# Kernel optimization log

Measured on AMD Instinct MI355X. Metric: run time of the kernel, lower is better.

## Reference

```python
import jax, jax.numpy as jnp
import numpy as np

B, C, H, W = 32, 3, 224, 224
P = 16
D = 768
NH = 12
HD = D // NH
DFF = 3072
L = 12
MAXLEN = 256
S = (H // P) * (W // P)  # 196 patches
EPS = 1e-5


def setup_inputs() -> dict:
    key = jax.random.key(0)
    ks = jax.random.split(key, 10)
    r = lambda k, shp, s=0.02: jax.random.normal(k, shp, jnp.float32) * s
    return {
        "x": jax.random.normal(ks[0], (B, C, H, W), jnp.float32),
        "bn_gamma": jnp.ones((C,), jnp.float32),
        "bn_beta": jnp.zeros((C,), jnp.float32),
        "bn_mean": jnp.zeros((C,), jnp.float32),
        "bn_var": jnp.ones((C,), jnp.float32),
        "proj_w": r(ks[1], (P * P * 3, D)),
        "proj_b": jnp.zeros((D,), jnp.float32),
        "cls_w": r(ks[2], (1, D)),
        "Wq": r(ks[3], (L, D, D)),
        "Wk": r(ks[4], (L, D, D)),
        "Wv": r(ks[5], (L, D, D)),
        "fc1_w": r(ks[6], (L, D, DFF)),
        "fc1_b": jnp.zeros((L, DFF), jnp.float32),
        "fc2_w": r(ks[7], (L, DFF, D)),
        "fc2_b": jnp.zeros((L, D), jnp.float32),
        "ln1_g": jnp.ones((L, D), jnp.float32),
        "ln1_b": jnp.zeros((L, D), jnp.float32),
        "ln2_g": jnp.ones((L, D), jnp.float32),
        "ln2_b": jnp.zeros((L, D), jnp.float32),
    }


def _pos_encoding(max_len, d):
    # Faithful to source: exponent is 2*i/d where i is the EVEN index itself.
    pos = jnp.arange(max_len, dtype=jnp.float32)[:, None]
    i = jnp.arange(0, d, 2, dtype=jnp.float32)[None, :]
    ang = pos / (10000.0 ** (2.0 * i / d))
    pe = jnp.zeros((max_len, d), jnp.float32)
    pe = pe.at[:, 0::2].set(jnp.sin(ang))
    pe = pe.at[:, 1::2].set(jnp.cos(ang))
    return pe


def _layernorm(x, g, b):
    m = jnp.mean(x, axis=-1, keepdims=True)
    v = jnp.mean((x - m) ** 2, axis=-1, keepdims=True)
    return (x - m) * jax.lax.rsqrt(v + EPS) * g + b


def reference(x, bn_gamma, bn_beta, bn_mean, bn_var, proj_w, proj_b, cls_w,
              Wq, Wk, Wv, fc1_w, fc1_b, fc2_w, fc2_b,
              ln1_g, ln1_b, ln2_g, ln2_b):
    b = x.shape[0]
    # BatchNorm2d (inference mode, running stats)
    xb = (x - bn_mean[None, :, None, None]) * jax.lax.rsqrt(bn_var[None, :, None, None] + EPS)
    xb = xb * bn_gamma[None, :, None, None] + bn_beta[None, :, None, None]
    # Patchify (nn.Unfold order: channel-major within each patch) -> [B, S, C*P*P]
    patches = xb.reshape(b, C, H // P, P, W // P, P)
    patches = patches.transpose(0, 2, 4, 1, 3, 5).reshape(b, S, C * P * P)
    h = patches @ proj_w + proj_b  # [B, S, D]
    cls = jnp.broadcast_to(cls_w[None], (b, 1, D))
    h = jnp.concatenate([cls, h], axis=1)  # [B, S+1, D]
    pe = _pos_encoding(MAXLEN, D)
    h = h + pe[None, : S + 1, :]
    scale = 1.0 / jnp.sqrt(jnp.float32(HD))
    n = S + 1
    for l in range(L):
        q = (h @ Wq[l]).reshape(b, n, NH, HD).transpose(0, 2, 1, 3)
        k = (h @ Wk[l]).reshape(b, n, NH, HD).transpose(0, 2, 1, 3)
        v = (h @ Wv[l]).reshape(b, n, NH, HD).transpose(0, 2, 1, 3)
        scores = jnp.einsum("bhqd,bhkd->bhqk", q, k) * scale
        attn = jax.nn.softmax(scores, axis=-1)
        att = jnp.einsum("bhqk,bhkd->bhqd", attn, v)  # [B, NH, n, HD]
        # Source bug replicated: direct view [B,NH,n,HD] -> [B,n,D] (no head transpose)
        att = att.reshape(b, n, D)
        h1 = _layernorm(h + att, ln1_g[l], ln1_b[l])
        ff = jax.nn.relu(h1 @ fc1_w[l] + fc1_b[l]) @ fc2_w[l] + fc2_b[l]
        h = _layernorm(h1 + ff, ln2_g[l], ln2_b[l])
    return h[:, 0, :]
```

## Files before the change

### kernel.cpp

```cpp
#include <hip/hip_runtime.h>

typedef unsigned short u16;
typedef unsigned int u32;
typedef __bf16 bf16x8 __attribute__((ext_vector_type(8)));
typedef float f32x4 __attribute__((ext_vector_type(4)));
typedef u16 u16x8 __attribute__((ext_vector_type(8)));

#define NB 32
#define ND 768
#define NTOK 197
#define NROWS (NB * NTOK)
#define NPATCH 196
#define PROWS (NB * NPATCH)
#define NHD 12
#define NDFF 3072
#define NLAY 12
#define NQKV 2304

static __device__ __forceinline__ u16 f2b(float f) {
  u32 u = __builtin_bit_cast(u32, f);
  u32 r = u + 0x7FFFu + ((u >> 16) & 1u);
  return (u16)(r >> 16);
}
static __device__ __forceinline__ float b2f(u16 u) {
  u32 x = ((u32)u) << 16;
  return __builtin_bit_cast(float, x);
}

static __device__ __forceinline__ float wsum(float v) {
#pragma unroll
  for (int off = 32; off > 0; off >>= 1) v += __shfl_xor(v, off);
  return v;
}

static __device__ __forceinline__ void stage16(const u16* g, u16* l) {
  __builtin_amdgcn_global_load_lds((const __attribute__((address_space(1))) void*)g,
                                   (__attribute__((address_space(3))) void*)l, 16, 0, 0);
}

__global__ void pe_kernel(float* __restrict__ pe) {
  int idx = blockIdx.x * 256 + threadIdx.x;
  if (idx >= NTOK * ND) return;
  int t = idx / ND, d = idx % ND;
  int i = d & ~1;
  float e = (2.0f * (float)i) / (float)ND;
  float denom = powf(10000.0f, e);
  float ang = (float)t / denom;
  pe[idx] = (d & 1) ? cosf(ang) : sinf(ang);
}

__global__ void patch_kernel(const float* __restrict__ x,
                             const float* __restrict__ bng, const float* __restrict__ bnb,
                             const float* __restrict__ bnm, const float* __restrict__ bnv,
                             u16* __restrict__ out) {
  int idx = blockIdx.x * 256 + threadIdx.x;
  if (idx >= PROWS * 96) return;
  int row = idx / 96, c8 = (idx % 96) * 8;
  int b = row / NPATCH, s = row % NPATCH;
  int ph = s / 14, pw = s % 14;
  int c = c8 / 256, rr = c8 % 256;
  int py = rr / 16, px0 = rr % 16;
  const float* xp =
      x + (((size_t)(b * 3 + c) * 224) + ph * 16 + py) * 224 + pw * 16 + px0;
  float scale = rsqrtf(bnv[c] + 1e-5f) * bng[c];
  float sub = bnm[c], add = bnb[c];
  u16x8 o;
#pragma unroll
  for (int j = 0; j < 8; j++) o[j] = f2b((xp[j] - sub) * scale + add);
  *reinterpret_cast<u16x8*>(out + (size_t)idx * 8) = o;
}

__global__ void cls_kernel(const float* __restrict__ cls_w, const float* __restrict__ pe,
                           u16* __restrict__ hb) {
  int idx = blockIdx.x * 256 + threadIdx.x;
  if (idx >= NB * ND) return;
  int b = idx / ND, d = idx % ND;
  hb[(size_t)(b * NTOK) * ND + d] = f2b(cls_w[d] + pe[d]);
}

__global__ __launch_bounds__(256) void transpose_cvt(const float* __restrict__ src,
                                                     u16* __restrict__ dst, int R, int C) {
  __shared__ float tile[32][33];
  int tx = threadIdx.x, ty = threadIdx.y;
  int c0 = blockIdx.x * 32, r0 = blockIdx.y * 32;
#pragma unroll
  for (int i = ty; i < 32; i += 8) {
    int r = r0 + i, c = c0 + tx;
    tile[i][tx] = (r < R && c < C) ? src[(size_t)r * C + c] : 0.f;
  }
  __syncthreads();
#pragma unroll
  for (int i = ty; i < 32; i += 8) {
    int c = c0 + i, r = r0 + tx;
    if (r < R && c < C) dst[(size_t)c * R + r] = f2b(tile[tx][i]);
  }
}

__global__ __launch_bounds__(512) void transpose_layer(
    const float* __restrict__ Wq, const float* __restrict__ Wk, const float* __restrict__ Wv,
    const float* __restrict__ f1, const float* __restrict__ f2,
    u16* __restrict__ wqkvt, u16* __restrict__ fc1t, u16* __restrict__ fc2t) {
  int idx = blockIdx.x;
  const float* src;
  u16* dst;
  int C, R, rt, ct;
  if (idx < 432) {
    int z = idx / 144, loc = idx % 144;
    src = z == 0 ? Wq : (z == 1 ? Wk : Wv);
    dst = wqkvt + (size_t)z * ND * ND;
    R = 768; C = 768; rt = loc / 12; ct = loc % 12;
  } else if (idx < 1008) {
    int loc = idx - 432;
    src = f1; dst = fc1t; R = 768; C = 3072; rt = loc / 48; ct = loc % 48;
  } else {
    int loc = idx - 1008;
    src = f2; dst = fc2t; R = 3072; C = 768; rt = loc / 12; ct = loc % 12;
  }
  __shared__ float tile[64][65];
  const int l2 = threadIdx.x & 31, rp = threadIdx.x >> 5;
  const int r0 = rt * 64, c0 = ct * 64;
#pragma unroll
  for (int i = rp; i < 64; i += 16) {
    float2 v = *reinterpret_cast<const float2*>(src + (size_t)(r0 + i) * C + c0 + l2 * 2);
    tile[i][l2 * 2] = v.x;
    tile[i][l2 * 2 + 1] = v.y;
  }
  __syncthreads();
#pragma unroll
  for (int j = rp; j < 64; j += 16) {
    u32 o = (u32)f2b(tile[l2 * 2][j]) | ((u32)f2b(tile[l2 * 2 + 1][j]) << 16);
    *reinterpret_cast<u32*>(dst + (size_t)(c0 + j) * R + r0 + l2 * 2) = o;
  }
}

template <int MODE>
__global__ __launch_bounds__(512, 4) void gemm2(const u16* __restrict__ A,
                                                const u16* __restrict__ Bt,
                                                const float* __restrict__ bias,
                                                const float* __restrict__ pe,
                                                u16* __restrict__ Cb,
                                                int M, int N, int K, int lda, int nby) {
  __shared__ u16 smem[36864];
  const int tid = threadIdx.x;
  const int w = tid >> 6, l = tid & 63;
  const int lr = l & 15, lg = l >> 4;
  const int wr = w >> 1, wc = w & 1;

  const int nwg = gridDim.x;
  const int q8 = nwg >> 3, r8 = nwg & 7;
  const int xcd = blockIdx.x & 7, sidx = blockIdx.x >> 3;
  const int swz = (xcd < r8 ? xcd * (q8 + 1) : r8 * (q8 + 1) + (xcd - r8) * q8) + sidx;
  const int m0 = (swz / nby) * 256, n0 = (swz % nby) * 128;

  A += (size_t)blockIdx.z * K;
  Bt += (size_t)blockIdx.z * K;

  const int srow = l >> 2;
  const int scol = (((l & 3) ^ ((l >> 2) & 3) ^ ((l >> 4) & 3))) * 8;
  int raA0 = m0 + 32 * w + srow;
  int raA1 = raA0 + 16;
  raA0 = raA0 < M ? raA0 : M - 1;
  raA1 = raA1 < M ? raA1 : M - 1;
  const int rbB = n0 + 16 * w + srow;
  const u16* pA0 = A + (size_t)raA0 * lda + scol;
  const u16* pA1 = A + (size_t)raA1 * lda + scol;
  const u16* pB = Bt + (size_t)rbB * lda + scol;
  const int dsgA0 = (2 * w) * 512;
  const int dsgA1 = (2 * w + 1) * 512;
  const int dsgB = 8192 + w * 512;

  const int xo = ((lg ^ (lr & 3) ^ ((lr >> 2) & 3))) * 8;
  const int aoff = (wr * 64 + lr) * 32 + xo;
  const int boff = 8192 + (wc * 64 + lr) * 32 + xo;

  f32x4 acc[4][4] = {};
  const int nk = K >> 5;

#define BARF                           \
  {                                    \
    __builtin_amdgcn_sched_barrier(0); \
    __builtin_amdgcn_s_barrier();      \
    asm volatile("" ::: "memory");     \
    __builtin_amdgcn_sched_barrier(0); \
  }
#define VMW(N) asm volatile("s_waitcnt vmcnt(" #N ")" ::: "memory");

  stage16(pA0, smem + dsgA0);
  stage16(pA1, smem + dsgA1);
  stage16(pB, smem + dsgB);
  stage16(pA0 + 32, smem + 12288 + dsgA0);
  stage16(pA1 + 32, smem + 12288 + dsgA1);
  stage16(pB + 32, smem + 12288 + dsgB);
  VMW(3);
  BARF;

  int cur = 0;
  for (int t = 0; t < nk; ++t) {
    const u16* sb = smem + cur * 12288;
    int c2 = cur + 2;
    if (c2 >= 3) c2 -= 3;
    const bool more2 = (t + 2) < nk;
    if (more2) {
      u16* db = smem + c2 * 12288;
      const int ko = (t + 2) * 32;
      stage16(pA0 + ko, db + dsgA0);
      stage16(pA1 + ko, db + dsgA1);
      stage16(pB + ko, db + dsgB);
    }
    bf16x8 ar[4], br[4];
#pragma unroll
    for (int n = 0; n < 4; ++n) br[n] = *(const bf16x8*)(sb + boff + n * 512);
#pragma unroll
    for (int m = 0; m < 4; ++m) ar[m] = *(const bf16x8*)(sb + aoff + m * 512);
    __builtin_amdgcn_s_setprio(1);
#pragma unroll
    for (int m = 0; m < 4; ++m) {
#pragma unroll
      for (int n = 0; n < 4; ++n)
        acc[m][n] = __builtin_amdgcn_mfma_f32_16x16x32_bf16(ar[m], br[n], acc[m][n], 0, 0, 0);
    }
    __builtin_amdgcn_s_setprio(0);
    if (more2) {
      VMW(3);
    } else if (t + 1 < nk) {
      VMW(0);
    }
    if (t + 1 < nk) BARF;
    cur = cur == 2 ? 0 : cur + 1;
  }

  const size_t zoff = (size_t)blockIdx.z * (size_t)M * (size_t)N;
#pragma unroll
  for (int m = 0; m < 4; ++m) {
    const int rowb = m0 + wr * 64 + m * 16 + lg * 4;
#pragma unroll
    for (int n = 0; n < 4; ++n) {
      const int col = n0 + wc * 64 + n * 16 + lr;
      float bval = (MODE == 0 || MODE == 2) ? bias[col] : 0.f;
#pragma unroll
      for (int r = 0; r < 4; ++r) {
        const int row = rowb + r;
        if (row < M) {
          float v = acc[m][n][r] + bval;
          if (MODE == 2) v = fmaxf(v, 0.f);
          if (MODE == 0) {
            int b = row / NPATCH, t = 1 + row % NPATCH;
            float val = v + pe[(size_t)t * ND + col];
            Cb[(size_t)(b * NTOK + t) * ND + col] = f2b(val);
          } else if (MODE == 4) {
            Cb[zoff + (size_t)row * N + col] = f2b(v);
          } else {
            Cb[(size_t)row * N + col] = f2b(v);
          }
        }
      }
    }
  }
}

__global__ __launch_bounds__(256) void attn_kernel(const u16* __restrict__ qkv,
                                                   u16* __restrict__ att) {
  const int b = blockIdx.x, h = blockIdx.y;
  const int tid = threadIdx.x;
  const int wave = tid >> 6, lane = tid & 63;
  const int lr = lane & 15, lg = lane >> 4;
  __shared__ u16 Vt[64][232];
  __shared__ u16 Pl[4][16][232];

  const size_t bbase = (size_t)(b * NTOK) * NQKV + h * 64;

  for (int idx = tid; idx < NTOK * 8; idx += 256) {
    int k2 = idx >> 3, d0 = (idx & 7) * 8;
    u16x8 v = *reinterpret_cast<const u16x8*>(qkv + bbase + (size_t)k2 * NQKV + 1536 + d0);
#pragma unroll
    for (int j = 0; j < 8; j++) Vt[d0 + j][k2] = v[j];
  }
  for (int idx = tid; idx < 64 * 35; idx += 256) {
    int d = idx / 35, k2 = 197 + idx % 35;
    Vt[d][k2] = 0;
  }
  for (int idx = tid; idx < 4 * 16 * 24; idx += 256) {
    int w = idx / (16 * 24), rr = (idx / 24) % 16, c = 208 + idx % 24;
    Pl[w][rr][c] = 0;
  }
  __syncthreads();

  for (int mt = wave; mt < 13; mt += 4) {
    int qrow = mt * 16 + lr;
    if (qrow > 196) qrow = 196;
    bf16x8 af[2];
#pragma unroll
    for (int ks = 0; ks < 2; ks++)
      af[ks] =
          *reinterpret_cast<const bf16x8*>(qkv + bbase + (size_t)qrow * NQKV + ks * 32 + lg * 8);

    f32x4 sf[13];
#pragma unroll
    for (int nt = 0; nt < 13; nt++) {
      int krow = nt * 16 + lr;
      if (krow > 196) krow = 196;
      f32x4 z = {0.f, 0.f, 0.f, 0.f};
#pragma unroll
      for (int ks = 0; ks < 2; ks++) {
        bf16x8 bf_ = *reinterpret_cast<const bf16x8*>(qkv + bbase + (size_t)krow * NQKV + 768 +
                                                      ks * 32 + lg * 8);
        z = __builtin_amdgcn_mfma_f32_16x16x32_bf16(af[ks], bf_, z, 0, 0, 0);
      }
      sf[nt] = z;
    }

    float sm[4];
#pragma unroll
    for (int r = 0; r < 4; r++) {
      float mx = -1e30f;
#pragma unroll
      for (int nt = 0; nt < 13; nt++) {
        int col = nt * 16 + lr;
        float val = (col < NTOK) ? sf[nt][r] * 0.125f : -1e30f;
        sf[nt][r] = val;
        mx = fmaxf(mx, val);
      }
#pragma unroll
      for (int off = 1; off < 16; off <<= 1) mx = fmaxf(mx, __shfl_xor(mx, off));
      float sum = 0.f;
#pragma unroll
      for (int nt = 0; nt < 13; nt++) {
        float pv = __expf(sf[nt][r] - mx);
        sum += pv;
        Pl[wave][lg * 4 + r][nt * 16 + lr] = f2b(pv);
      }
#pragma unroll
      for (int off = 1; off < 16; off <<= 1) sum += __shfl_xor(sum, off);
      sm[r] = sum;
    }

#pragma unroll
    for (int dt = 0; dt < 4; dt++) {
      f32x4 o = {0.f, 0.f, 0.f, 0.f};
#pragma unroll
      for (int ks = 0; ks < 7; ks++) {
        bf16x8 pa = *reinterpret_cast<const bf16x8*>(&Pl[wave][lr][ks * 32 + lg * 8]);
        bf16x8 vv = *reinterpret_cast<const bf16x8*>(&Vt[dt * 16 + lr][ks * 32 + lg * 8]);
        o = __builtin_amdgcn_mfma_f32_16x16x32_bf16(pa, vv, o, 0, 0, 0);
      }
#pragma unroll
      for (int r = 0; r < 4; r++) {
        int q = mt * 16 + lg * 4 + r;
        if (q < NTOK)
          att[(size_t)b * (NTOK * ND) + ((size_t)(h * NTOK + q)) * 64 + dt * 16 + lr] =
              f2b(o[r] / sm[r]);
      }
    }
  }
}

__global__ __launch_bounds__(384) void ln_kernel(const u16* __restrict__ xa,
                                                 const u16* __restrict__ xb,
                                                 const float* __restrict__ gw,
                                                 const float* __restrict__ bw,
                                                 u16* __restrict__ yb) {
  int row = blockIdx.x, tid = threadIdx.x;
  size_t p2 = (size_t)row * 384 + tid;
  u32 aa = reinterpret_cast<const u32*>(xa)[p2];
  u32 bb = reinterpret_cast<const u32*>(xb)[p2];
  float v0 = b2f((u16)(aa & 0xffff)) + b2f((u16)(bb & 0xffff));
  float v1 = b2f((u16)(aa >> 16)) + b2f((u16)(bb >> 16));
  __shared__ float red[8], red2[8];
  float s = wsum(v0 + v1);
  if ((tid & 63) == 0) red[tid >> 6] = s;
  __syncthreads();
  float mean = (red[0] + red[1] + red[2] + red[3] + red[4] + red[5]) * (1.f / 768.f);
  float d0 = v0 - mean, d1 = v1 - mean;
  float q = wsum(d0 * d0 + d1 * d1);
  if ((tid & 63) == 0) red2[tid >> 6] = q;
  __syncthreads();
  float inv =
      rsqrtf((red2[0] + red2[1] + red2[2] + red2[3] + red2[4] + red2[5]) * (1.f / 768.f) + 1e-5f);
  int d = tid * 2;
  float o0 = d0 * inv * gw[d] + bw[d];
  float o1 = d1 * inv * gw[d + 1] + bw[d + 1];
  reinterpret_cast<u32*>(yb)[p2] = (u32)f2b(o0) | ((u32)f2b(o1) << 16);
}

__global__ __launch_bounds__(384) void ln_fuse2(const u16* __restrict__ h1b,
                                                const u16* __restrict__ parts,
                                                const float* __restrict__ fb,
                                                const float* __restrict__ gw,
                                                const float* __restrict__ bw,
                                                u16* __restrict__ yb) {
  const size_t PS2 = (size_t)NROWS * ND / 2;
  int row = blockIdx.x, tid = threadIdx.x;
  size_t p2 = (size_t)row * 384 + tid;
  u32 aa = reinterpret_cast<const u32*>(h1b)[p2];
  const u32* pp = reinterpret_cast<const u32*>(parts);
  u32 q0 = pp[p2], q1 = pp[PS2 + p2], q2 = pp[2 * PS2 + p2];
  int d = tid * 2;
  float v0 = b2f((u16)(aa & 0xffff)) + b2f((u16)(q0 & 0xffff)) + b2f((u16)(q1 & 0xffff)) +
             b2f((u16)(q2 & 0xffff)) + fb[d];
  float v1 = b2f((u16)(aa >> 16)) + b2f((u16)(q0 >> 16)) + b2f((u16)(q1 >> 16)) +
             b2f((u16)(q2 >> 16)) + fb[d + 1];
  __shared__ float red[8], red2[8];
  float s = wsum(v0 + v1);
  if ((tid & 63) == 0) red[tid >> 6] = s;
  __syncthreads();
  float mean = (red[0] + red[1] + red[2] + red[3] + red[4] + red[5]) * (1.f / 768.f);
  float d0 = v0 - mean, d1 = v1 - mean;
  float q = wsum(d0 * d0 + d1 * d1);
  if ((tid & 63) == 0) red2[tid >> 6] = q;
  __syncthreads();
  float inv =
      rsqrtf((red2[0] + red2[1] + red2[2] + red2[3] + red2[4] + red2[5]) * (1.f / 768.f) + 1e-5f);
  float o0 = d0 * inv * gw[d] + bw[d];
  float o1 = d1 * inv * gw[d + 1] + bw[d + 1];
  reinterpret_cast<u32*>(yb)[p2] = (u32)f2b(o0) | ((u32)f2b(o1) << 16);
}

__global__ void outcopy_kernel(const u16* __restrict__ hb, float* __restrict__ out) {
  int idx = blockIdx.x * 256 + threadIdx.x;
  if (idx >= NB * ND) return;
  int b = idx / ND, d = idx % ND;
  out[idx] = b2f(hb[(size_t)(b * NTOK) * ND + d]);
}

extern "C" void kernel_launch(void* const* d_in, const int* in_sizes, int n_in, void* d_out,
                              int out_size, void* d_ws, size_t ws_size, hipStream_t stream) {
  const float* x = (const float*)d_in[0];
  const float* bng = (const float*)d_in[1];
  const float* bnb = (const float*)d_in[2];
  const float* bnm = (const float*)d_in[3];
  const float* bnv = (const float*)d_in[4];
  const float* proj_w = (const float*)d_in[5];
  const float* proj_b = (const float*)d_in[6];
  const float* cls_w = (const float*)d_in[7];
  const float* Wq = (const float*)d_in[8];
  const float* Wk = (const float*)d_in[9];
  const float* Wv = (const float*)d_in[10];
  const float* fc1_w = (const float*)d_in[11];
  const float* fc1_b = (const float*)d_in[12];
  const float* fc2_w = (const float*)d_in[13];
  const float* fc2_b = (const float*)d_in[14];
  const float* ln1_g = (const float*)d_in[15];
  const float* ln1_b = (const float*)d_in[16];
  const float* ln2_g = (const float*)d_in[17];
  const float* ln2_b = (const float*)d_in[18];

  char* wp = (char*)d_ws;
  auto carve = [&](size_t bytes) -> char* {
    char* r = wp;
    wp += (bytes + 255) & ~(size_t)255;
    return r;
  };
  float* pe = (float*)carve((size_t)NTOK * ND * 4);
  u16* patches = (u16*)carve((size_t)PROWS * ND * 2);
  u16* projwt = (u16*)carve((size_t)ND * ND * 2);
  u16* wqkvt = (u16*)carve((size_t)NQKV * ND * 2);
  u16* fc1t = (u16*)carve((size_t)ND * NDFF * 2);
  u16* fc2t = (u16*)carve((size_t)ND * NDFF * 2);
  u16* hb = (u16*)carve((size_t)NROWS * ND * 2);
  u16* h1b = (u16*)carve((size_t)NROWS * ND * 2);
  char* uni = carve(3 * (size_t)NROWS * ND * 2);
  u16* qkvb = (u16*)uni;
  u16* parts = (u16*)uni;
  u16* att = (u16*)carve((size_t)NROWS * ND * 2);
  u16* ffb = (u16*)carve((size_t)NROWS * NDFF * 2);
  if ((size_t)(wp - (char*)d_ws) > ws_size) return;

  pe_kernel<<<(NTOK * ND + 255) / 256, 256, 0, stream>>>(pe);
  patch_kernel<<<(PROWS * 96 + 255) / 256, 256, 0, stream>>>(x, bng, bnb, bnm, bnv, patches);
  transpose_cvt<<<dim3(24, 24), dim3(32, 8), 0, stream>>>(proj_w, projwt, ND, ND);
  gemm2<0><<<dim3(150, 1, 1), 512, 0, stream>>>(patches, projwt, proj_b, pe, hb, PROWS, ND, ND,
                                                ND, 6);
  cls_kernel<<<(NB * ND + 255) / 256, 256, 0, stream>>>(cls_w, pe, hb);

  for (int l = 0; l < NLAY; ++l) {
    size_t wo = (size_t)l * ND * ND;
    transpose_layer<<<1584, 512, 0, stream>>>(Wq + wo, Wk + wo, Wv + wo,
                                              fc1_w + (size_t)l * ND * NDFF,
                                              fc2_w + (size_t)l * NDFF * ND, wqkvt, fc1t, fc2t);
    gemm2<1><<<dim3(450, 1, 1), 512, 0, stream>>>(hb, wqkvt, nullptr, nullptr, qkvb, NROWS, NQKV,
                                                  ND, ND, 18);
    attn_kernel<<<dim3(NB, NHD), 256, 0, stream>>>(qkvb, att);
    ln_kernel<<<NROWS, 384, 0, stream>>>(hb, att, ln1_g + l * ND, ln1_b + l * ND, h1b);
    gemm2<2><<<dim3(600, 1, 1), 512, 0, stream>>>(h1b, fc1t, fc1_b + l * NDFF, nullptr, ffb,
                                                  NROWS, NDFF, ND, ND, 24);
    gemm2<4><<<dim3(150, 1, 3), 512, 0, stream>>>(ffb, fc2t, nullptr, nullptr, parts, NROWS, ND,
                                                  1024, NDFF, 6);
    ln_fuse2<<<NROWS, 384, 0, stream>>>(h1b, parts, fc2_b + l * ND, ln2_g + l * ND, ln2_b + l * ND,
                                        hb);
  }
  outcopy_kernel<<<(NB * ND + 255) / 256, 256, 0, stream>>>(hb, (float*)d_out);
}
```

Before: 2.218 ms.

## Fold next-layer weight transpose into QKV GEMM grid and use wave-per-row layernorm

The per-layer weight transpose/convert kernel becomes extra workgroups appended to the QKV GEMM launch, which prepare the next layer's weights into a double-buffered set. This removes one launch per layer and lets transpose work overlap GEMM tail occupancy. Both layernorm kernels now give each 64-lane wave a whole row, so block-level shared-memory reductions and barriers go away. The cost is twice the workspace for transposed weights, and the transpose blocks compete with GEMM blocks for the same CUs.

```diff
diff --git a/kernel.cpp b/kernel.cpp
--- a/kernel.cpp
+++ b/kernel.cpp
@@ -96,11 +96,11 @@
   }
 }
 
-__global__ __launch_bounds__(512) void transpose_layer(
-    const float* __restrict__ Wq, const float* __restrict__ Wk, const float* __restrict__ Wv,
-    const float* __restrict__ f1, const float* __restrict__ f2,
-    u16* __restrict__ wqkvt, u16* __restrict__ fc1t, u16* __restrict__ fc2t) {
-  int idx = blockIdx.x;
+static __device__ __forceinline__ void transpose_body(
+    int idx, const float* __restrict__ Wq, const float* __restrict__ Wk,
+    const float* __restrict__ Wv, const float* __restrict__ f1, const float* __restrict__ f2,
+    u16* __restrict__ wqkvt, u16* __restrict__ fc1t, u16* __restrict__ fc2t, void* smemraw,
+    int tid) {
   const float* src;
   u16* dst;
   int C, R, rt, ct;
@@ -116,8 +116,8 @@
     int loc = idx - 1008;
     src = f2; dst = fc2t; R = 3072; C = 768; rt = loc / 12; ct = loc % 12;
   }
-  __shared__ float tile[64][65];
-  const int l2 = threadIdx.x & 31, rp = threadIdx.x >> 5;
+  float(*tile)[65] = (float(*)[65])smemraw;
+  const int l2 = tid & 31, rp = tid >> 5;
   const int r0 = rt * 64, c0 = ct * 64;
 #pragma unroll
   for (int i = rp; i < 64; i += 16) {
@@ -133,20 +133,33 @@
   }
 }
 
-template <int MODE>
-__global__ __launch_bounds__(512, 4) void gemm2(const u16* __restrict__ A,
-                                                const u16* __restrict__ Bt,
-                                                const float* __restrict__ bias,
-                                                const float* __restrict__ pe,
-                                                u16* __restrict__ Cb,
-                                                int M, int N, int K, int lda, int nby) {
+__global__ __launch_bounds__(512) void transpose_layer(
+    const float* __restrict__ Wq, const float* __restrict__ Wk, const float* __restrict__ Wv,
+    const float* __restrict__ f1, const float* __restrict__ f2,
+    u16* __restrict__ wqkvt, u16* __restrict__ fc1t, u16* __restrict__ fc2t) {
+  __shared__ float tile[64][65];
+  transpose_body(blockIdx.x, Wq, Wk, Wv, f1, f2, wqkvt, fc1t, fc2t, tile, threadIdx.x);
+}
+
+template <int MODE, bool TR>
+__global__ __launch_bounds__(512, 4) void gemm2(
+    const u16* __restrict__ A, const u16* __restrict__ Bt, const float* __restrict__ bias,
+    const float* __restrict__ pe, u16* __restrict__ Cb, int M, int N, int K, int lda, int nby,
+    int ngx, const float* __restrict__ tWq, const float* __restrict__ tWk,
+    const float* __restrict__ tWv, const float* __restrict__ tf1, const float* __restrict__ tf2,
+    u16* __restrict__ twqkv, u16* __restrict__ tfc1, u16* __restrict__ tfc2) {
   __shared__ u16 smem[36864];
+  if (TR && (int)blockIdx.x >= ngx) {
+    transpose_body(blockIdx.x - ngx, tWq, tWk, tWv, tf1, tf2, twqkv, tfc1, tfc2, smem,
+                   threadIdx.x);
+    return;
+  }
   const int tid = threadIdx.x;
   const int w = tid >> 6, l = tid & 63;
   const int lr = l & 15, lg = l >> 4;
   const int wr = w >> 1, wc = w & 1;
 
-  const int nwg = gridDim.x;
+  const int nwg = ngx;
   const int q8 = nwg >> 3, r8 = nwg & 7;
   const int xcd = blockIdx.x & 7, sidx = blockIdx.x >> 3;
   const int swz = (xcd < r8 ? xcd * (q8 + 1) : r8 * (q8 + 1) + (xcd - r8) * q8) + sidx;
@@ -354,65 +367,90 @@
   }
 }
 
-__global__ __launch_bounds__(384) void ln_kernel(const u16* __restrict__ xa,
+__global__ __launch_bounds__(256) void ln_kernel(const u16* __restrict__ xa,
                                                  const u16* __restrict__ xb,
                                                  const float* __restrict__ gw,
                                                  const float* __restrict__ bw,
                                                  u16* __restrict__ yb) {
-  int row = blockIdx.x, tid = threadIdx.x;
-  size_t p2 = (size_t)row * 384 + tid;
-  u32 aa = reinterpret_cast<const u32*>(xa)[p2];
-  u32 bb = reinterpret_cast<const u32*>(xb)[p2];
-  float v0 = b2f((u16)(aa & 0xffff)) + b2f((u16)(bb & 0xffff));
-  float v1 = b2f((u16)(aa >> 16)) + b2f((u16)(bb >> 16));
-  __shared__ float red[8], red2[8];
-  float s = wsum(v0 + v1);
-  if ((tid & 63) == 0) red[tid >> 6] = s;
-  __syncthreads();
-  float mean = (red[0] + red[1] + red[2] + red[3] + red[4] + red[5]) * (1.f / 768.f);
-  float d0 = v0 - mean, d1 = v1 - mean;
-  float q = wsum(d0 * d0 + d1 * d1);
-  if ((tid & 63) == 0) red2[tid >> 6] = q;
-  __syncthreads();
-  float inv =
-      rsqrtf((red2[0] + red2[1] + red2[2] + red2[3] + red2[4] + red2[5]) * (1.f / 768.f) + 1e-5f);
-  int d = tid * 2;
-  float o0 = d0 * inv * gw[d] + bw[d];
-  float o1 = d1 * inv * gw[d + 1] + bw[d + 1];
-  reinterpret_cast<u32*>(yb)[p2] = (u32)f2b(o0) | ((u32)f2b(o1) << 16);
-}
-
-__global__ __launch_bounds__(384) void ln_fuse2(const u16* __restrict__ h1b,
+  int row = blockIdx.x * 4 + (threadIdx.x >> 6);
+  int lane = threadIdx.x & 63;
+  size_t base = (size_t)row * 384;
+  float v0[6], v1[6];
+  float s = 0.f;
+#pragma unroll
+  for (int i = 0; i < 6; i++) {
+    size_t j = base + lane + 64 * i;
+    u32 aa = reinterpret_cast<const u32*>(xa)[j];
+    u32 bb = reinterpret_cast<const u32*>(xb)[j];
+    v0[i] = b2f((u16)(aa & 0xffff)) + b2f((u16)(bb & 0xffff));
+    v1[i] = b2f((u16)(aa >> 16)) + b2f((u16)(bb >> 16));
+    s += v0[i] + v1[i];
+  }
+  s = wsum(s);
+  float mean = s * (1.f / 768.f);
+  float q = 0.f;
+#pragma unroll
+  for (int i = 0; i < 6; i++) {
+    float d0 = v0[i] - mean, d1 = v1[i] - mean;
+    q += d0 * d0 + d1 * d1;
+  }
+  q = wsum(q);
+  float inv = rsqrtf(q * (1.f / 768.f) + 1e-5f);
+#pragma unroll
+  for (int i = 0; i < 6; i++) {
+    int j = lane + 64 * i;
+    float2 g = reinterpret_cast<const float2*>(gw)[j];
+    float2 bb = reinterpret_cast<const float2*>(bw)[j];
+    float o0 = (v0[i] - mean) * inv * g.x + bb.x;
+    float o1 = (v1[i] - mean) * inv * g.y + bb.y;
+    reinterpret_cast<u32*>(yb)[base + j] = (u32)f2b(o0) | ((u32)f2b(o1) << 16);
+  }
+}
+
+__global__ __launch_bounds__(256) void ln_fuse2(const u16* __restrict__ h1b,
                                                 const u16* __restrict__ parts,
                                                 const float* __restrict__ fb,
                                                 const float* __restrict__ gw,
                                                 const float* __restrict__ bw,
                                                 u16* __restrict__ yb) {
   const size_t PS2 = (size_t)NROWS * ND / 2;
-  int row = blockIdx.x, tid = threadIdx.x;
-  size_t p2 = (size_t)row * 384 + tid;
-  u32 aa = reinterpret_cast<const u32*>(h1b)[p2];
-  const u32* pp = reinterpret_cast<const u32*>(parts);
-  u32 q0 = pp[p2], q1 = pp[PS2 + p2], q2 = pp[2 * PS2 + p2];
-  int d = tid * 2;
-  float v0 = b2f((u16)(aa & 0xffff)) + b2f((u16)(q0 & 0xffff)) + b2f((u16)(q1 & 0xffff)) +
-             b2f((u16)(q2 & 0xffff)) + fb[d];
-  float v1 = b2f((u16)(aa >> 16)) + b2f((u16)(q0 >> 16)) + b2f((u16)(q1 >> 16)) +
-             b2f((u16)(q2 >> 16)) + fb[d + 1];
-  __shared__ float red[8], red2[8];
-  float s = wsum(v0 + v1);
-  if ((tid & 63) == 0) red[tid >> 6] = s;
-  __syncthreads();
-  float mean = (red[0] + red[1] + red[2] + red[3] + red[4] + red[5]) * (1.f / 768.f);
-  float d0 = v0 - mean, d1 = v1 - mean;
-  float q = wsum(d0 * d0 + d1 * d1);
-  if ((tid & 63) == 0) red2[tid >> 6] = q;
-  __syncthreads();
-  float inv =
-      rsqrtf((red2[0] + red2[1] + red2[2] + red2[3] + red2[4] + red2[5]) * (1.f / 768.f) + 1e-5f);
-  float o0 = d0 * inv * gw[d] + bw[d];
-  float o1 = d1 * inv * gw[d + 1] + bw[d + 1];
-  reinterpret_cast<u32*>(yb)[p2] = (u32)f2b(o0) | ((u32)f2b(o1) << 16);
+  int row = blockIdx.x * 4 + (threadIdx.x >> 6);
+  int lane = threadIdx.x & 63;
+  size_t base = (size_t)row * 384;
+  float v0[6], v1[6];
+  float s = 0.f;
+#pragma unroll
+  for (int i = 0; i < 6; i++) {
+    size_t j = base + lane + 64 * i;
+    u32 aa = reinterpret_cast<const u32*>(h1b)[j];
+    const u32* pp = reinterpret_cast<const u32*>(parts);
+    u32 q0 = pp[j], q1 = pp[PS2 + j], q2 = pp[2 * PS2 + j];
+    float2 fbv = reinterpret_cast<const float2*>(fb)[lane + 64 * i];
+    v0[i] = b2f((u16)(aa & 0xffff)) + b2f((u16)(q0 & 0xffff)) + b2f((u16)(q1 & 0xffff)) +
+            b2f((u16)(q2 & 0xffff)) + fbv.x;
+    v1[i] = b2f((u16)(aa >> 16)) + b2f((u16)(q0 >> 16)) + b2f((u16)(q1 >> 16)) +
+            b2f((u16)(q2 >> 16)) + fbv.y;
+    s += v0[i] + v1[i];
+  }
+  s = wsum(s);
+  float mean = s * (1.f / 768.f);
+  float q = 0.f;
+#pragma unroll
+  for (int i = 0; i < 6; i++) {
+    float d0 = v0[i] - mean, d1 = v1[i] - mean;
+    q += d0 * d0 + d1 * d1;
+  }
+  q = wsum(q);
+  float inv = rsqrtf(q * (1.f / 768.f) + 1e-5f);
+#pragma unroll
+  for (int i = 0; i < 6; i++) {
+    int j = lane + 64 * i;
+    float2 g = reinterpret_cast<const float2*>(gw)[j];
+    float2 bb = reinterpret_cast<const float2*>(bw)[j];
+    float o0 = (v0[i] - mean) * inv * g.x + bb.x;
+    float o1 = (v1[i] - mean) * inv * g.y + bb.y;
+    reinterpret_cast<u32*>(yb)[base + j] = (u32)f2b(o0) | ((u32)f2b(o1) << 16);
+  }
 }
 
 __global__ void outcopy_kernel(const u16* __restrict__ hb, float* __restrict__ out) {
@@ -453,9 +491,9 @@
   float* pe = (float*)carve((size_t)NTOK * ND * 4);
   u16* patches = (u16*)carve((size_t)PROWS * ND * 2);
   u16* projwt = (u16*)carve((size_t)ND * ND * 2);
-  u16* wqkvt = (u16*)carve((size_t)NQKV * ND * 2);
-  u16* fc1t = (u16*)carve((size_t)ND * NDFF * 2);
-  u16* fc2t = (u16*)carve((size_t)ND * NDFF * 2);
+  u16* wqkvt[2] = {(u16*)carve((size_t)NQKV * ND * 2), (u16*)carve((size_t)NQKV * ND * 2)};
+  u16* fc1t[2] = {(u16*)carve((size_t)ND * NDFF * 2), (u16*)carve((size_t)ND * NDFF * 2)};
+  u16* fc2t[2] = {(u16*)carve((size_t)ND * NDFF * 2), (u16*)carve((size_t)ND * NDFF * 2)};
   u16* hb = (u16*)carve((size_t)NROWS * ND * 2);
   u16* h1b = (u16*)carve((size_t)NROWS * ND * 2);
   char* uni = carve(3 * (size_t)NROWS * ND * 2);
@@ -468,25 +506,33 @@
   pe_kernel<<<(NTOK * ND + 255) / 256, 256, 0, stream>>>(pe);
   patch_kernel<<<(PROWS * 96 + 255) / 256, 256, 0, stream>>>(x, bng, bnb, bnm, bnv, patches);
   transpose_cvt<<<dim3(24, 24), dim3(32, 8), 0, stream>>>(proj_w, projwt, ND, ND);
-  gemm2<0><<<dim3(150, 1, 1), 512, 0, stream>>>(patches, projwt, proj_b, pe, hb, PROWS, ND, ND,
-                                                ND, 6);
+  gemm2<0, false><<<dim3(150, 1, 1), 512, 0, stream>>>(
+      patches, projwt, proj_b, pe, hb, PROWS, ND, ND, ND, 6, 150, nullptr, nullptr, nullptr,
+      nullptr, nullptr, nullptr, nullptr, nullptr);
   cls_kernel<<<(NB * ND + 255) / 256, 256, 0, stream>>>(cls_w, pe, hb);
+  transpose_layer<<<1584, 512, 0, stream>>>(Wq, Wk, Wv, fc1_w, fc2_w, wqkvt[0], fc1t[0],
+                                            fc2t[0]);
 
   for (int l = 0; l < NLAY; ++l) {
-    size_t wo = (size_t)l * ND * ND;
-    transpose_layer<<<1584, 512, 0, stream>>>(Wq + wo, Wk + wo, Wv + wo,
-                                              fc1_w + (size_t)l * ND * NDFF,
-                                              fc2_w + (size_t)l * NDFF * ND, wqkvt, fc1t, fc2t);
-    gemm2<1><<<dim3(450, 1, 1), 512, 0, stream>>>(hb, wqkvt, nullptr, nullptr, qkvb, NROWS, NQKV,
-                                                  ND, ND, 18);
+    const int cur = l & 1, nxt = cur ^ 1;
+    const bool more = l + 1 < NLAY;
+    size_t nwo = (size_t)(l + 1) * ND * ND;
+    size_t nfo = (size_t)(l + 1) * ND * NDFF;
+    gemm2<1, true><<<dim3(450 + (more ? 1584 : 0), 1, 1), 512, 0, stream>>>(
+        hb, wqkvt[cur], nullptr, nullptr, qkvb, NROWS, NQKV, ND, ND, 18, 450,
+        more ? Wq + nwo : nullptr, more ? Wk + nwo : nullptr, more ? Wv + nwo : nullptr,
+        more ? fc1_w + nfo : nullptr, more ? fc2_w + nfo : nullptr, wqkvt[nxt], fc1t[nxt],
+        fc2t[nxt]);
     attn_kernel<<<dim3(NB, NHD), 256, 0, stream>>>(qkvb, att);
-    ln_kernel<<<NROWS, 384, 0, stream>>>(hb, att, ln1_g + l * ND, ln1_b + l * ND, h1b);
-    gemm2<2><<<dim3(600, 1, 1), 512, 0, stream>>>(h1b, fc1t, fc1_b + l * NDFF, nullptr, ffb,
-                                                  NROWS, NDFF, ND, ND, 24);
-    gemm2<4><<<dim3(150, 1, 3), 512, 0, stream>>>(ffb, fc2t, nullptr, nullptr, parts, NROWS, ND,
-                                                  1024, NDFF, 6);
-    ln_fuse2<<<NROWS, 384, 0, stream>>>(h1b, parts, fc2_b + l * ND, ln2_g + l * ND, ln2_b + l * ND,
-                                        hb);
+    ln_kernel<<<NROWS / 4, 256, 0, stream>>>(hb, att, ln1_g + l * ND, ln1_b + l * ND, h1b);
+    gemm2<2, false><<<dim3(600, 1, 1), 512, 0, stream>>>(
+        h1b, fc1t[cur], fc1_b + l * NDFF, nullptr, ffb, NROWS, NDFF, ND, ND, 24, 600, nullptr,
+        nullptr, nullptr, nullptr, nullptr, nullptr, nullptr, nullptr);
+    gemm2<4, false><<<dim3(150, 1, 3), 512, 0, stream>>>(
+        ffb, fc2t[cur], nullptr, nullptr, parts, NROWS, ND, 1024, NDFF, 6, 150, nullptr, nullptr,
+        nullptr, nullptr, nullptr, nullptr, nullptr, nullptr);
+    ln_fuse2<<<NROWS / 4, 256, 0, stream>>>(h1b, parts, fc2_b + l * ND, ln2_g + l * ND,
+                                            ln2_b + l * ND, hb);
   }
   outcopy_kernel<<<(NB * ND + 255) / 256, 256, 0, stream>>>(hb, (float*)d_out);
 }
```

New measurement: 2.108 ms. -5.0%, faster.
